# Kernel tuning notes

Hardware: AMD Instinct MI355X
Metric: run time of the kernel (lower is better)

## Reference

```python
import jax, jax.numpy as jnp
import numpy as np

ND, NT, B = 16384, 16384, 4096
FD, FT, C = 256, 256, 768


def _gat(x_src, x_dst, ei, Ws, Wd, a_s, a_d, b, num_dst, self_loops):
    """PyG GATConv, heads=1: per-edge attention softmax over incoming edges."""
    if self_loops:
        loops = jnp.arange(num_dst, dtype=ei.dtype)
        ei = jnp.concatenate([ei, jnp.stack([loops, loops])], axis=1)
    src, dst = ei[0], ei[1]
    hs = x_src @ Ws                                   # [Ns, C]
    hd = x_dst @ Wd                                   # [Ndst, C]
    e = jax.nn.leaky_relu((hs @ a_s)[src] + (hd @ a_d)[dst], 0.2)   # [E]
    m = jax.ops.segment_max(e, dst, num_segments=num_dst)
    p = jnp.exp(e - m[dst])
    s = jax.ops.segment_sum(p, dst, num_segments=num_dst)
    alpha = p / (s[dst] + 1e-16)
    out = jax.ops.segment_sum(hs[src] * alpha[:, None], dst, num_segments=num_dst)
    return out + b


def _l2norm(x):
    n = jnp.linalg.norm(x, axis=1, keepdims=True)
    return x / jnp.maximum(n, 1e-12)


def setup_inputs() -> dict:
    ks = iter(jax.random.split(jax.random.key(0), 64))
    def nrm(shape, fan_in=None):
        s = 1.0 if fan_in is None else (1.0 / fan_in) ** 0.5
        return jax.random.normal(next(ks), shape, jnp.float32) * s
    inp = {}
    inp["x_drug"] = nrm((ND, FD))
    inp["x_target"] = nrm((NT, FT))
    inp["cell_features"] = nrm((B, 890))
    for et, fs, fd in (("dd", FD, FD), ("dt", FD, FT), ("tt", FT, FT)):
        inp[f"W_src_{et}"] = nrm((fs, C), fs)
        inp[f"W_dst_{et}"] = nrm((fd, C), fd)
        inp[f"a_src_{et}"] = nrm((C,), C)
        inp[f"a_dst_{et}"] = nrm((C,), C)
        inp[f"b_{et}"] = jnp.zeros((C,), jnp.float32)
    for name, fi, fo in (("red1", 890, 2048), ("red2", 2048, 512), ("red3", 512, 2 * C),
                         ("r2a", 4 * C, 2048), ("r2b", 2048, 512), ("r2c", 512, C), ("cls", C, 2)):
        inp[f"{name}_w"] = nrm((fi, fo), fi)
        inp[f"{name}_b"] = jnp.zeros((fo,), jnp.float32)
    inp["drug1_id"] = jax.random.randint(next(ks), (B,), 0, ND)
    inp["drug2_id"] = jax.random.randint(next(ks), (B,), 0, ND)
    inp["ei_dd"] = jax.random.randint(next(ks), (2, 131072), 0, ND)
    inp["ei_dt"] = jnp.stack([jax.random.randint(next(ks), (262144,), 0, ND),
                              jax.random.randint(next(ks), (262144,), 0, NT)])
    inp["ei_tt"] = jax.random.randint(next(ks), (2, 262144), 0, NT)
    return inp


def reference(x_drug, x_target, cell_features,
              W_src_dd, W_dst_dd, a_src_dd, a_dst_dd, b_dd,
              W_src_dt, W_dst_dt, a_src_dt, a_dst_dt, b_dt,
              W_src_tt, W_dst_tt, a_src_tt, a_dst_tt, b_tt,
              red1_w, red1_b, red2_w, red2_b, red3_w, red3_b,
              r2a_w, r2a_b, r2b_w, r2b_b, r2c_w, r2c_b,
              cls_w, cls_b,
              drug1_id, drug2_id, ei_dd, ei_dt, ei_tt):
    # HeteroConv (aggr='sum') followed by per-type ReLU, num_layers=1
    drug = jax.nn.relu(_gat(x_drug, x_drug, ei_dd,
                            W_src_dd, W_dst_dd, a_src_dd, a_dst_dd, b_dd, ND, True))
    target = jax.nn.relu(
        _gat(x_drug, x_target, ei_dt, W_src_dt, W_dst_dt, a_src_dt, a_dst_dt, b_dt, NT, False)
        + _gat(x_target, x_target, ei_tt, W_src_tt, W_dst_tt, a_src_tt, a_dst_tt, b_tt, NT, True))
    del target  # with num_layers=1 the target embeddings never feed the output (faithful)
    d1 = drug[drug1_id]
    d2 = drug[drug2_id]
    cell = _l2norm(cell_features)
    cell = jax.nn.relu(cell @ red1_w + red1_b)
    cell = jax.nn.relu(cell @ red2_w + red2_b)
    cell = jax.nn.relu(cell @ red3_w + red3_b)          # [B, 2*C]
    hidden = _l2norm(jnp.concatenate([d1, d2, cell], axis=1))  # [B, 4*C]
    hidden = jax.nn.relu(hidden @ r2a_w + r2a_b)
    hidden = jax.nn.relu(hidden @ r2b_w + r2b_b)
    hidden = jax.nn.relu(hidden @ r2c_w + r2c_b)
    return hidden @ cls_w + cls_b                       # [B, 2]
```

## Files before the change

kernel.cpp:

```cpp
#include <hip/hip_runtime.h>
#include <cstdint>

#define ND 16384
#define BATCH 4096
#define CDIM 768
#define E_DD 131072
#define FD 256

typedef unsigned short u16;
typedef u16 u16x4 __attribute__((ext_vector_type(4)));
typedef u16 u16x8 __attribute__((ext_vector_type(8)));
typedef short s16x8 __attribute__((ext_vector_type(8)));
typedef float f32x4 __attribute__((ext_vector_type(4)));

__device__ __forceinline__ u16 f2bf(float x) {
  union { float f; uint32_t u; } v; v.f = x;
  uint32_t r = v.u + 0x7fffu + ((v.u >> 16) & 1u);
  return (u16)(r >> 16);
}
__device__ __forceinline__ float bf2f(u16 h) {
  union { float f; uint32_t u; } v; v.u = ((uint32_t)h) << 16;
  return v.f;
}
__device__ __forceinline__ uint32_t split2p(float x) {
  u16 h = f2bf(x);
  u16 l = f2bf(x - bf2f(h));
  return ((uint32_t)h << 16) | l;
}

#define KP 40

template <int KS, int OUT_BF16, int RELU, int BIAS, int ASPLIT, int ALO, int BLO>
__device__ __forceinline__ void gemm_core(
    int bx, int by, int bz,
    const float* __restrict__ Af,
    const u16* __restrict__ Ahi, const u16* __restrict__ Alo,
    const u16* __restrict__ Bhi, const u16* __restrict__ Blo,
    const float* __restrict__ bias,
    float* __restrict__ Cf, u16* __restrict__ Chi,
    int M, int N, int K, u16* AsB, u16* BsB) {
  constexpr int MT = 4, NT = 4;
  constexpr int BM = 128, BN = 128;
  constexpr int ASEG = BM / 64;
  constexpr int BSEG = BN / 64;

  const int t = threadIdx.x;
  const int bm0 = bx * BM, bn0 = by * BN;
  const int wid = t >> 6, lane = t & 63;
  const int quad = lane >> 4, l16 = lane & 15;
  const int wm0 = (wid >> 1) * (MT * 16);
  const int wn0 = (wid & 1) * (NT * 16);

  const int chunk = K / KS;
  const int kbeg = (KS > 1) ? bz * chunk : 0;
  const int kend = kbeg + chunk;

  auto As = [&](int a, int r, int k) -> u16& { return AsB[(a * BM + r) * KP + k]; };
  auto Bs = [&](int a, int r, int k) -> u16& { return BsB[(a * BN + r) * KP + k]; };

  f32x4 acc[MT][NT];
#pragma unroll
  for (int i = 0; i < MT; ++i)
#pragma unroll
    for (int j = 0; j < NT; ++j) acc[i][j] = (f32x4){0.f, 0.f, 0.f, 0.f};

  u16x8 pAh[ASEG], pAl[ASEG], pBh[BSEG], pBl[BSEG];

  auto loadA = [&](int c, int kk) {
    int s = t + 256 * c, row = s >> 2, kq = (s & 3) * 8;
    size_t off = (size_t)(bm0 + row) * K + kk + kq;
    if (ASPLIT) {
      f32x4 v0 = *(const f32x4*)(Af + off);
      f32x4 v1 = *(const f32x4*)(Af + off + 4);
      u16x8 h, l;
#pragma unroll
      for (int e = 0; e < 4; ++e) {
        uint32_t p = split2p(v0[e]);
        h[e] = (u16)(p >> 16); l[e] = (u16)(p & 0xffffu);
        uint32_t q = split2p(v1[e]);
        h[e + 4] = (u16)(q >> 16); l[e + 4] = (u16)(q & 0xffffu);
      }
      pAh[c] = h; pAl[c] = l;
    } else {
      pAh[c] = *(const u16x8*)(Ahi + off);
      if (ALO) pAl[c] = *(const u16x8*)(Alo + off);
    }
  };
  auto loadB = [&](int c, int kk) {
    int s = t + 256 * c, row = s >> 2, kq = (s & 3) * 8;
    size_t off = (size_t)(bn0 + row) * K + kk + kq;
    pBh[c] = *(const u16x8*)(Bhi + off);
    if (BLO) pBl[c] = *(const u16x8*)(Blo + off);
  };

#pragma unroll
  for (int c = 0; c < ASEG; ++c) loadA(c, kbeg);
#pragma unroll
  for (int c = 0; c < BSEG; ++c) loadB(c, kbeg);

  for (int k0 = kbeg;;) {
    __syncthreads();
#pragma unroll
    for (int c = 0; c < ASEG; ++c) {
      int s = t + 256 * c, row = s >> 2, kq = (s & 3) * 8;
      *(u16x8*)&As(0, row, kq) = pAh[c];
      if (ALO) *(u16x8*)&As(1, row, kq) = pAl[c];
    }
#pragma unroll
    for (int c = 0; c < BSEG; ++c) {
      int s = t + 256 * c, row = s >> 2, kq = (s & 3) * 8;
      *(u16x8*)&Bs(0, row, kq) = pBh[c];
      if (BLO) *(u16x8*)&Bs(1, row, kq) = pBl[c];
    }
    __syncthreads();

    int kn = k0 + 32;
    if (kn < kend) {
#pragma unroll
      for (int c = 0; c < ASEG; ++c) loadA(c, kn);
#pragma unroll
      for (int c = 0; c < BSEG; ++c) loadB(c, kn);
    }

    s16x8 ah[MT], al[MT], bh[NT], bl[NT];
#pragma unroll
    for (int mi = 0; mi < MT; ++mi) {
      ah[mi] = *(const s16x8*)&As(0, wm0 + mi * 16 + l16, quad * 8);
      if (ALO) al[mi] = *(const s16x8*)&As(1, wm0 + mi * 16 + l16, quad * 8);
    }
#pragma unroll
    for (int ni = 0; ni < NT; ++ni) {
      bh[ni] = *(const s16x8*)&Bs(0, wn0 + ni * 16 + l16, quad * 8);
      if (BLO) bl[ni] = *(const s16x8*)&Bs(1, wn0 + ni * 16 + l16, quad * 8);
    }
#pragma unroll
    for (int mi = 0; mi < MT; ++mi)
#pragma unroll
      for (int ni = 0; ni < NT; ++ni) {
        acc[mi][ni] = __builtin_amdgcn_mfma_f32_16x16x32_bf16(
            ah[mi], bh[ni], acc[mi][ni], 0, 0, 0);
        if (BLO)
          acc[mi][ni] = __builtin_amdgcn_mfma_f32_16x16x32_bf16(
              ah[mi], bl[ni], acc[mi][ni], 0, 0, 0);
        if (ALO)
          acc[mi][ni] = __builtin_amdgcn_mfma_f32_16x16x32_bf16(
              al[mi], bh[ni], acc[mi][ni], 0, 0, 0);
      }
    k0 = kn;
    if (k0 >= kend) break;
  }

  float* Cp = (KS > 1) ? Cf + (size_t)bz * M * N : Cf;
#pragma unroll
  for (int mi = 0; mi < MT; ++mi) {
#pragma unroll
    for (int ni = 0; ni < NT; ++ni) {
      int row = bm0 + wm0 + mi * 16 + quad * 4;
      int col = bn0 + wn0 + ni * 16 + l16;
      float bv = BIAS ? bias[col] : 0.f;
#pragma unroll
      for (int r = 0; r < 4; ++r) {
        float v = acc[mi][ni][r] + bv;
        if (RELU) v = fmaxf(v, 0.f);
        size_t o = (size_t)(row + r) * N + col;
        if (OUT_BF16) Chi[o] = f2bf(v);
        else Cp[o] = v;
      }
    }
  }
}

template <int KS, int OUT_BF16, int RELU, int BIAS, int ASPLIT, int ALO, int BLO>
__global__ __launch_bounds__(256) void mfma_gemm(
    const float* __restrict__ Af,
    const u16* __restrict__ Ahi, const u16* __restrict__ Alo,
    const u16* __restrict__ Bhi, const u16* __restrict__ Blo,
    const float* __restrict__ bias,
    float* __restrict__ Cf, u16* __restrict__ Chi,
    int M, int N, int K) {
  __shared__ __align__(16) u16 AsB[(ALO ? 2 : 1) * 128 * KP];
  __shared__ __align__(16) u16 BsB[(BLO ? 2 : 1) * 128 * KP];
  gemm_core<KS, OUT_BF16, RELU, BIAS, ASPLIT, ALO, BLO>(
      blockIdx.x, blockIdx.y, (KS > 1) ? (int)blockIdx.z : 0,
      Af, Ahi, Alo, Bhi, Blo, bias, Cf, Chi, M, N, K, AsB, BsB);
}

__device__ __forceinline__ void gat_body(
    int idx, const u16* __restrict__ hs, const float* __restrict__ es,
    const float* __restrict__ ed, const int* __restrict__ offsets,
    const int* __restrict__ slots, const float* __restrict__ bias,
    const int* __restrict__ d1, const int* __restrict__ d2,
    u16* __restrict__ out) {
  if (idx >= 2 * BATCH) return;
  int d = (idx < BATCH) ? d1[idx] : d2[idx - BATCH];
  int lane = threadIdx.x & 63;
  int beg = offsets[d], end = offsets[d + 1];
  float edv = ed[d];
  float mx = -1e30f;
  for (int j = beg + lane; j < end; j += 64) {
    float e = es[slots[j]] + edv;
    e = e >= 0.f ? e : 0.2f * e;
    mx = fmaxf(mx, e);
  }
#pragma unroll
  for (int m = 32; m; m >>= 1) mx = fmaxf(mx, __shfl_xor(mx, m));
  float sm = 0.f;
  for (int j = beg + lane; j < end; j += 64) {
    float e = es[slots[j]] + edv;
    e = e >= 0.f ? e : 0.2f * e;
    sm += expf(e - mx);
  }
#pragma unroll
  for (int m = 32; m; m >>= 1) sm += __shfl_xor(sm, m);
  float inv = 1.f / (sm + 1e-16f);
  int c8 = lane * 8;
  int c4 = 512 + lane * 4;
  float a8[8] = {};
  float a4[4] = {};
  for (int j = beg; j < end; ++j) {
    int srcn = slots[j];
    float e = es[srcn] + edv;
    e = e >= 0.f ? e : 0.2f * e;
    float alpha = expf(e - mx) * inv;
    const u16* hrow = hs + (size_t)srcn * CDIM;
    u16x8 r8 = *(const u16x8*)(hrow + c8);
    u16x4 r4 = *(const u16x4*)(hrow + c4);
#pragma unroll
    for (int e2 = 0; e2 < 8; ++e2) a8[e2] = fmaf(alpha, bf2f(r8[e2]), a8[e2]);
#pragma unroll
    for (int e2 = 0; e2 < 4; ++e2) a4[e2] = fmaf(alpha, bf2f(r4[e2]), a4[e2]);
  }
  u16* orow = out + (size_t)d * CDIM;
  u16x8 o8;
  u16x4 o4;
#pragma unroll
  for (int e2 = 0; e2 < 8; ++e2) o8[e2] = f2bf(fmaxf(a8[e2] + bias[c8 + e2], 0.f));
#pragma unroll
  for (int e2 = 0; e2 < 4; ++e2) o4[e2] = f2bf(fmaxf(a4[e2] + bias[c4 + e2], 0.f));
  *(u16x8*)(orow + c8) = o8;
  *(u16x4*)(orow + c4) = o4;
}

__global__ __launch_bounds__(256) void dual_gemm_red1_hs(
    const u16* __restrict__ cn, const u16* __restrict__ r1T,
    const float* __restrict__ red1_b, u16* __restrict__ c1,
    const float* __restrict__ xd, const u16* __restrict__ wsrcT,
    u16* __restrict__ hs) {
  __shared__ __align__(16) u16 AsB[2 * 128 * KP];
  __shared__ __align__(16) u16 BsB[128 * KP];
  int b = blockIdx.x;
  if (b < 512) {
    gemm_core<1, 1, 1, 1, 0, 0, 0>(b & 31, b >> 5, 0, nullptr, cn, nullptr,
                                   r1T, nullptr, red1_b, nullptr, c1,
                                   BATCH, 2048, 896, AsB, BsB);
  } else {
    int b2 = b - 512;
    gemm_core<1, 1, 0, 0, 1, 1, 0>(b2 & 127, b2 >> 7, 0, xd, nullptr, nullptr,
                                   wsrcT, nullptr, nullptr, nullptr, hs,
                                   ND, CDIM, FD, AsB, BsB);
  }
}

__global__ __launch_bounds__(256) void dual_red2_gat(
    const u16* __restrict__ c1, const u16* __restrict__ r2T,
    float* __restrict__ P,
    const u16* __restrict__ hs, const float* __restrict__ es,
    const float* __restrict__ ed, const int* __restrict__ offsets,
    const int* __restrict__ slots, const float* __restrict__ bias,
    const int* __restrict__ d1, const int* __restrict__ d2,
    u16* __restrict__ drug) {
  __shared__ __align__(16) u16 AsB[128 * KP];
  __shared__ __align__(16) u16 BsB[128 * KP];
  int b = blockIdx.x;
  if (b < 512) {
    gemm_core<4, 0, 0, 0, 0, 0, 0>(b & 31, (b >> 5) & 3, b >> 7, nullptr,
                                   c1, nullptr, r2T, nullptr, nullptr, P,
                                   nullptr, BATCH, 512, 2048, AsB, BsB);
  } else {
    int idx = (b - 512) * 4 + (threadIdx.x >> 6);
    gat_body(idx, hs, es, ed, offsets, slots, bias, d1, d2, drug);
  }
}

template <int KS>
__global__ void reduce_split_ks(const float* __restrict__ P,
                                const float* __restrict__ bias,
                                u16* __restrict__ Chi, int M, int N) {
  int i = blockIdx.x * 256 + threadIdx.x;
  int total = (M * N) >> 2;
  if (i >= total) return;
  f32x4 s = ((const f32x4*)P)[i];
#pragma unroll
  for (int z = 1; z < KS; ++z) s += ((const f32x4*)P)[(size_t)z * total + i];
  int col = (i * 4) % N;
  f32x4 bv = *(const f32x4*)(bias + col);
  u16x4 h;
#pragma unroll
  for (int e = 0; e < 4; ++e) h[e] = f2bf(fmaxf(s[e] + bv[e], 0.f));
  *(u16x4*)&Chi[i * 4] = h;
}

__global__ void reduce_cls(const float* __restrict__ P,
                           const float* __restrict__ bias,
                           const float* __restrict__ clsw,
                           const float* __restrict__ clsb,
                           float* __restrict__ out) {
  int row = blockIdx.x * 4 + (threadIdx.x >> 6);
  int lane = threadIdx.x & 63;
  const f32x4* p0 = (const f32x4*)(P + (size_t)row * CDIM);
  const f32x4* p1 = (const f32x4*)(P + (size_t)BATCH * CDIM + (size_t)row * CDIM);
  float s0 = 0.f, s1 = 0.f;
#pragma unroll
  for (int i = 0; i < 3; ++i) {
    int c4 = lane + 64 * i;
    f32x4 a = p0[c4] + p1[c4];
    f32x4 bv = *(const f32x4*)(bias + c4 * 4);
#pragma unroll
    for (int e = 0; e < 4; ++e) {
      float h = fmaxf(a[e] + bv[e], 0.f);
      int c = c4 * 4 + e;
      s0 = fmaf(h, clsw[c * 2 + 0], s0);
      s1 = fmaf(h, clsw[c * 2 + 1], s1);
    }
  }
#pragma unroll
  for (int m = 32; m; m >>= 1) {
    s0 += __shfl_xor(s0, m);
    s1 += __shfl_xor(s1, m);
  }
  if (lane == 0) {
    out[row * 2 + 0] = s0 + clsb[0];
    out[row * 2 + 1] = s1 + clsb[1];
  }
}

struct TDesc {
  const float* W;
  u16* Th;
  int K, N, Kpad, start;
};
struct TPack { TDesc d[7]; };

__global__ void multi_transpose(TPack p) {
  __shared__ float tile[32][33];
  int b = blockIdx.x;
  int mi = 0;
#pragma unroll
  for (int i = 1; i < 7; ++i)
    if (b >= p.d[i].start) mi = i;
  TDesc dd = p.d[mi];
  int rel = b - dd.start;
  int tilesX = dd.Kpad / 32;
  int k0 = (rel % tilesX) * 32, n0 = (rel / tilesX) * 32;
  int tx = threadIdx.x, ty = threadIdx.y;
#pragma unroll
  for (int i = 0; i < 4; ++i) {
    int k = k0 + ty + 8 * i, n = n0 + tx;
    tile[ty + 8 * i][tx] = (k < dd.K && n < dd.N) ? dd.W[(size_t)k * dd.N + n] : 0.f;
  }
  __syncthreads();
#pragma unroll
  for (int i = 0; i < 4; ++i) {
    int n = n0 + ty + 8 * i, k = k0 + tx;
    if (n < dd.N) dd.Th[(size_t)n * dd.Kpad + k] = f2bf(tile[tx][ty + 8 * i]);
  }
}

__global__ void wvec_kernel(const float* __restrict__ Wsrc,
                            const float* __restrict__ Wdst,
                            const float* __restrict__ a_s,
                            const float* __restrict__ a_d,
                            float* __restrict__ wsv, float* __restrict__ wdv) {
  int k = blockIdx.x;
  int t = threadIdx.x;
  __shared__ float rs[256], rd[256];
  float s = 0.f, d = 0.f;
  for (int c = t; c < CDIM; c += 256) {
    s += Wsrc[(size_t)k * CDIM + c] * a_s[c];
    d += Wdst[(size_t)k * CDIM + c] * a_d[c];
  }
  rs[t] = s; rd[t] = d;
  __syncthreads();
  for (int st = 128; st; st >>= 1) {
    if (t < st) { rs[t] += rs[t + st]; rd[t] += rd[t + st]; }
    __syncthreads();
  }
  if (t == 0) { wsv[k] = rs[0]; wdv[k] = rd[0]; }
}

__global__ void esed_kernel(const float* __restrict__ x,
                            const float* __restrict__ wsv,
                            const float* __restrict__ wdv,
                            float* __restrict__ es, float* __restrict__ ed,
                            int* __restrict__ counts) {
  if (blockIdx.x < 64) counts[blockIdx.x * 256 + threadIdx.x] = 1;
  int i = blockIdx.x * 256 + threadIdx.x;
  int lane = threadIdx.x & 63;
  int row = i >> 6;
  int c4 = lane * 4;
  f32x4 v = ((const f32x4*)x)[i];
  f32x4 ws = *(const f32x4*)(wsv + c4);
  f32x4 wd = *(const f32x4*)(wdv + c4);
  float a = v[0] * ws[0] + v[1] * ws[1] + v[2] * ws[2] + v[3] * ws[3];
  float b = v[0] * wd[0] + v[1] * wd[1] + v[2] * wd[2] + v[3] * wd[3];
#pragma unroll
  for (int m = 32; m; m >>= 1) {
    a += __shfl_xor(a, m);
    b += __shfl_xor(b, m);
  }
  if (lane == 0) { es[row] = a; ed[row] = b; }
}

__global__ void count_edges(const int* __restrict__ dst, int* counts) {
  int e = blockIdx.x * 256 + threadIdx.x;
  if (e < E_DD) atomicAdd(&counts[dst[e]], 1);
}
__global__ void scan_kernel(const int* __restrict__ counts, int* __restrict__ offsets,
                            int* __restrict__ cursor, int* __restrict__ slots) {
  __shared__ int part[512];
  int t = threadIdx.x;
  int base = t * 32;
  int s = 0;
  for (int i = 0; i < 32; ++i) s += counts[base + i];
  part[t] = s;
  __syncthreads();
  if (t == 0) {
    int run = 0;
    for (int i = 0; i < 512; ++i) { int tmp = part[i]; part[i] = run; run += tmp; }
    offsets[ND] = run;
  }
  __syncthreads();
  int run = part[t];
  for (int i = 0; i < 32; ++i) {
    int d = base + i;
    offsets[d] = run;
    slots[run] = d;
    cursor[d] = run + 1;
    run += counts[d];
  }
}
__global__ void scatter_edges(const int* __restrict__ src, const int* __restrict__ dst,
                              int* cursor, int* slots) {
  int e = blockIdx.x * 256 + threadIdx.x;
  if (e < E_DD) {
    int pos = atomicAdd(&cursor[dst[e]], 1);
    slots[pos] = src[e];
  }
}

__global__ void l2norm_bf16(const float* __restrict__ in, u16* __restrict__ hi,
                            int L, int Lp) {
  int row = blockIdx.x;
  int t = threadIdx.x;
  __shared__ float red[256];
  const float* irow = in + (size_t)row * L;
  float s = 0.f;
  for (int c = t; c < L; c += 256) { float v = irow[c]; s += v * v; }
  red[t] = s;
  __syncthreads();
  for (int st = 128; st; st >>= 1) {
    if (t < st) red[t] += red[t + st];
    __syncthreads();
  }
  float inv = 1.f / fmaxf(sqrtf(red[0]), 1e-12f);
  for (int c = t; c < Lp; c += 256) {
    float v = (c < L) ? irow[c] * inv : 0.f;
    hi[(size_t)row * Lp + c] = f2bf(v);
  }
}

__global__ __launch_bounds__(256) void hidden_build_bf16(
    const u16* __restrict__ drug, const u16* __restrict__ c3,
    const int* __restrict__ d1, const int* __restrict__ d2,
    u16* __restrict__ hhi) {
  int row = blockIdx.x;
  int t = threadIdx.x;
  const u16* s1 = drug + (size_t)d1[row] * CDIM;
  const u16* s2 = drug + (size_t)d2[row] * CDIM;
  const u16* s3 = c3 + (size_t)row * (2 * CDIM);
  float vals[12];
  float ss = 0.f;
#pragma unroll
  for (int i = 0; i < 12; ++i) {
    int c = t + 256 * i;
    float v;
    if (i < 3)      v = bf2f(s1[c]);
    else if (i < 6) v = bf2f(s2[c - CDIM]);
    else            v = bf2f(s3[c - 2 * CDIM]);
    vals[i] = v;
    ss += v * v;
  }
  __shared__ float red[256];
  red[t] = ss;
  __syncthreads();
  for (int st = 128; st; st >>= 1) {
    if (t < st) red[t] += red[t + st];
    __syncthreads();
  }
  float inv = 1.f / fmaxf(sqrtf(red[0]), 1e-12f);
  u16* hrow_h = hhi + (size_t)row * (4 * CDIM);
#pragma unroll
  for (int i = 0; i < 12; ++i) hrow_h[t + 256 * i] = f2bf(vals[i] * inv);
}

extern "C" void kernel_launch(void* const* d_in, const int* in_sizes, int n_in,
                              void* d_out, int out_size, void* d_ws, size_t ws_size,
                              hipStream_t stream) {
  const float* x_drug   = (const float*)d_in[0];
  const float* cellf    = (const float*)d_in[2];
  const float* W_src_dd = (const float*)d_in[3];
  const float* W_dst_dd = (const float*)d_in[4];
  const float* a_src_dd = (const float*)d_in[5];
  const float* a_dst_dd = (const float*)d_in[6];
  const float* b_dd     = (const float*)d_in[7];
  const float* red1_w = (const float*)d_in[18];
  const float* red1_b = (const float*)d_in[19];
  const float* red2_w = (const float*)d_in[20];
  const float* red2_b = (const float*)d_in[21];
  const float* red3_w = (const float*)d_in[22];
  const float* red3_b = (const float*)d_in[23];
  const float* r2a_w  = (const float*)d_in[24];
  const float* r2a_b  = (const float*)d_in[25];
  const float* r2b_w  = (const float*)d_in[26];
  const float* r2b_b  = (const float*)d_in[27];
  const float* r2c_w  = (const float*)d_in[28];
  const float* r2c_b  = (const float*)d_in[29];
  const float* cls_w  = (const float*)d_in[30];
  const float* cls_b  = (const float*)d_in[31];
  const int* drug1_id = (const int*)d_in[32];
  const int* drug2_id = (const int*)d_in[33];
  const int* ei_dd    = (const int*)d_in[34];
  float* out = (float*)d_out;

  const int* dd_src = ei_dd;
  const int* dd_dst = ei_dd + E_DD;

  char* w = (char*)d_ws;
  size_t off = 0;
  auto alloc = [&](size_t bytes) -> char* {
    char* p = w + off;
    off = (off + bytes + 255) & ~(size_t)255;
    return p;
  };
  u16* hs   = (u16*)alloc((size_t)ND * CDIM * 2);
  u16* drug = (u16*)alloc((size_t)ND * CDIM * 2);
  u16* c3   = (u16*)alloc((size_t)BATCH * 2 * CDIM * 2);
  float* P  = (float*)alloc((size_t)4 * BATCH * 512 * 4);
  u16* hid_hi = hs;
  u16* cn_hi = (u16*)alloc((size_t)BATCH * 896 * 2);
  u16* c1_hi = (u16*)alloc((size_t)BATCH * 2048 * 2);
  u16* c2_hi = (u16*)alloc((size_t)BATCH * 512 * 2);
  u16* wsrcT_hi = (u16*)alloc((size_t)CDIM * FD * 2);
  u16* r1T_hi = (u16*)alloc((size_t)2048 * 896 * 2);
  u16* r2T_hi = (u16*)alloc((size_t)512 * 2048 * 2);
  u16* r3T_hi = (u16*)alloc((size_t)1536 * 512 * 2);
  u16* raT_hi = (u16*)alloc((size_t)2048 * 3072 * 2);
  u16* rbT_hi = (u16*)alloc((size_t)512 * 2048 * 2);
  u16* rcT_hi = (u16*)alloc((size_t)768 * 512 * 2);
  float* es  = (float*)alloc((size_t)ND * 4);
  float* ed  = (float*)alloc((size_t)ND * 4);
  float* wsv = (float*)alloc(FD * 4);
  float* wdv = (float*)alloc(FD * 4);
  int* counts  = (int*)alloc((size_t)ND * 4);
  int* offsets = (int*)alloc((size_t)(ND + 1) * 4);
  int* cursor  = (int*)alloc((size_t)ND * 4);
  int* slots   = (int*)alloc((size_t)(E_DD + ND) * 4);
  (void)ws_size; (void)n_in; (void)in_sizes; (void)out_size;

  TPack tp;
  tp.d[0] = {W_src_dd, wsrcT_hi, 256, 768, 256, 0};
  tp.d[1] = {red1_w, r1T_hi, 890, 2048, 896, 192};
  tp.d[2] = {red2_w, r2T_hi, 2048, 512, 2048, 1984};
  tp.d[3] = {red3_w, r3T_hi, 512, 1536, 512, 3008};
  tp.d[4] = {r2a_w, raT_hi, 3072, 2048, 3072, 3776};
  tp.d[5] = {r2b_w, rbT_hi, 2048, 512, 2048, 9920};
  tp.d[6] = {r2c_w, rcT_hi, 512, 768, 512, 10944};
  multi_transpose<<<11328, dim3(32, 8), 0, stream>>>(tp);

  wvec_kernel<<<FD, 256, 0, stream>>>(W_src_dd, W_dst_dd, a_src_dd, a_dst_dd, wsv, wdv);
  esed_kernel<<<ND * FD / 1024, 256, 0, stream>>>(x_drug, wsv, wdv, es, ed, counts);
  count_edges<<<E_DD / 256, 256, 0, stream>>>(dd_dst, counts);
  scan_kernel<<<1, 512, 0, stream>>>(counts, offsets, cursor, slots);
  scatter_edges<<<E_DD / 256, 256, 0, stream>>>(dd_src, dd_dst, cursor, slots);
  l2norm_bf16<<<BATCH, 256, 0, stream>>>(cellf, cn_hi, 890, 896);

  dual_gemm_red1_hs<<<1280, 256, 0, stream>>>(cn_hi, r1T_hi, red1_b, c1_hi,
                                              x_drug, wsrcT_hi, hs);

  dual_red2_gat<<<512 + 2 * BATCH / 4, 256, 0, stream>>>(
      c1_hi, r2T_hi, P, hs, es, ed, offsets, slots, b_dd, drug1_id, drug2_id, drug);
  reduce_split_ks<4><<<BATCH * 512 / 1024, 256, 0, stream>>>(P, red2_b, c2_hi, BATCH, 512);
  mfma_gemm<1, 1, 1, 1, 0, 0, 0><<<dim3(BATCH / 128, 1536 / 128), 256, 0, stream>>>(
      nullptr, c2_hi, nullptr, r3T_hi, nullptr, red3_b, nullptr, c3, BATCH, 1536, 512);

  hidden_build_bf16<<<BATCH, 256, 0, stream>>>(drug, c3, drug1_id, drug2_id, hid_hi);

  mfma_gemm<1, 1, 1, 1, 0, 0, 0><<<dim3(BATCH / 128, 2048 / 128), 256, 0, stream>>>(
      nullptr, hid_hi, nullptr, raT_hi, nullptr, r2a_b, nullptr, c1_hi, BATCH, 2048, 3072);
  mfma_gemm<4, 0, 0, 0, 0, 0, 0><<<dim3(BATCH / 128, 512 / 128, 4), 256, 0, stream>>>(
      nullptr, c1_hi, nullptr, rbT_hi, nullptr, nullptr, P, nullptr, BATCH, 512, 2048);
  reduce_split_ks<4><<<BATCH * 512 / 1024, 256, 0, stream>>>(P, r2b_b, c2_hi, BATCH, 512);
  mfma_gemm<2, 0, 0, 0, 0, 0, 0><<<dim3(BATCH / 128, CDIM / 128, 2), 256, 0, stream>>>(
      nullptr, c2_hi, nullptr, rcT_hi, nullptr, nullptr, P, nullptr, BATCH, CDIM, 512);
  reduce_cls<<<BATCH / 4, 256, 0, stream>>>(P, r2c_b, cls_w, cls_b, out);
}
```

Measured before the change: 493.9 us.

## Deduplicate gathered drug ids for GAT and fuse small prep kernels

Marks which drug nodes are referenced by drug1_id/drug2_id, compacts them into a unique list with an atomic counter, and runs the GAT aggregation only once per unique node instead of once per batch slot. This removes duplicated edge softmax and aggregation work. It also merges several small launches: the wvec reduction into the transpose kernel, the esed and l2norm work into one kernel, and the edge count and scatter steps with the mask and compaction passes. The cost is extra mask/list buffers and atomics, and the GAT grid is still sized for the worst case, so idle waves exit early.

```diff
diff --git a/kernel.cpp b/kernel.cpp
--- a/kernel.cpp
+++ b/kernel.cpp
@@ -189,10 +189,10 @@
     int idx, const u16* __restrict__ hs, const float* __restrict__ es,
     const float* __restrict__ ed, const int* __restrict__ offsets,
     const int* __restrict__ slots, const float* __restrict__ bias,
-    const int* __restrict__ d1, const int* __restrict__ d2,
+    const int* __restrict__ list, const int* __restrict__ cnt,
     u16* __restrict__ out) {
-  if (idx >= 2 * BATCH) return;
-  int d = (idx < BATCH) ? d1[idx] : d2[idx - BATCH];
+  if (idx >= *cnt) return;
+  int d = list[idx];
   int lane = threadIdx.x & 63;
   int beg = offsets[d], end = offsets[d + 1];
   float edv = ed[d];
@@ -267,7 +267,7 @@
     const u16* __restrict__ hs, const float* __restrict__ es,
     const float* __restrict__ ed, const int* __restrict__ offsets,
     const int* __restrict__ slots, const float* __restrict__ bias,
-    const int* __restrict__ d1, const int* __restrict__ d2,
+    const int* __restrict__ list, const int* __restrict__ cnt,
     u16* __restrict__ drug) {
   __shared__ __align__(16) u16 AsB[128 * KP];
   __shared__ __align__(16) u16 BsB[128 * KP];
@@ -278,7 +278,7 @@
                                    nullptr, BATCH, 512, 2048, AsB, BsB);
   } else {
     int idx = (b - 512) * 4 + (threadIdx.x >> 6);
-    gat_body(idx, hs, es, ed, offsets, slots, bias, d1, d2, drug);
+    gat_body(idx, hs, es, ed, offsets, slots, bias, list, cnt, drug);
   }
 }
 
@@ -341,9 +341,30 @@
 };
 struct TPack { TDesc d[7]; };
 
-__global__ void multi_transpose(TPack p) {
+__global__ __launch_bounds__(256) void transpose_wvec(
+    TPack p, const float* __restrict__ Wsrc, const float* __restrict__ Wdst,
+    const float* __restrict__ a_s, const float* __restrict__ a_d,
+    float* __restrict__ wsv, float* __restrict__ wdv) {
   __shared__ float tile[32][33];
+  __shared__ float rs[256], rd[256];
   int b = blockIdx.x;
+  int t = threadIdx.x;
+  if (b >= 11328) {
+    int k = b - 11328;
+    float s = 0.f, d = 0.f;
+    for (int c = t; c < CDIM; c += 256) {
+      s += Wsrc[(size_t)k * CDIM + c] * a_s[c];
+      d += Wdst[(size_t)k * CDIM + c] * a_d[c];
+    }
+    rs[t] = s; rd[t] = d;
+    __syncthreads();
+    for (int st = 128; st; st >>= 1) {
+      if (t < st) { rs[t] += rs[t + st]; rd[t] += rd[t + st]; }
+      __syncthreads();
+    }
+    if (t == 0) { wsv[k] = rs[0]; wdv[k] = rd[0]; }
+    return;
+  }
   int mi = 0;
 #pragma unroll
   for (int i = 1; i < 7; ++i)
@@ -352,7 +373,7 @@
   int rel = b - dd.start;
   int tilesX = dd.Kpad / 32;
   int k0 = (rel % tilesX) * 32, n0 = (rel / tilesX) * 32;
-  int tx = threadIdx.x, ty = threadIdx.y;
+  int tx = t & 31, ty = t >> 5;
 #pragma unroll
   for (int i = 0; i < 4; ++i) {
     int k = k0 + ty + 8 * i, n = n0 + tx;
@@ -366,55 +387,70 @@
   }
 }
 
-__global__ void wvec_kernel(const float* __restrict__ Wsrc,
-                            const float* __restrict__ Wdst,
-                            const float* __restrict__ a_s,
-                            const float* __restrict__ a_d,
-                            float* __restrict__ wsv, float* __restrict__ wdv) {
-  int k = blockIdx.x;
+__global__ __launch_bounds__(256) void prep_act(
+    const float* __restrict__ x, const float* __restrict__ wsv,
+    const float* __restrict__ wdv, float* __restrict__ es,
+    float* __restrict__ ed, int* __restrict__ counts, int* __restrict__ mask,
+    int* __restrict__ cnt,
+    const float* __restrict__ cellf, u16* __restrict__ cn) {
+  __shared__ float red[256];
+  int b = blockIdx.x;
   int t = threadIdx.x;
-  __shared__ float rs[256], rd[256];
-  float s = 0.f, d = 0.f;
-  for (int c = t; c < CDIM; c += 256) {
-    s += Wsrc[(size_t)k * CDIM + c] * a_s[c];
-    d += Wdst[(size_t)k * CDIM + c] * a_d[c];
-  }
-  rs[t] = s; rd[t] = d;
-  __syncthreads();
-  for (int st = 128; st; st >>= 1) {
-    if (t < st) { rs[t] += rs[t + st]; rd[t] += rd[t + st]; }
+  if (b < 4096) {
+    if (b < 64) {
+      int i = b * 256 + t;
+      counts[i] = 1;
+      mask[i] = 0;
+      if (i == 0) *cnt = 0;
+    }
+    int i = b * 256 + t;
+    int lane = t & 63;
+    int row = i >> 6;
+    int c4 = lane * 4;
+    f32x4 v = ((const f32x4*)x)[i];
+    f32x4 ws = *(const f32x4*)(wsv + c4);
+    f32x4 wd = *(const f32x4*)(wdv + c4);
+    float a = v[0] * ws[0] + v[1] * ws[1] + v[2] * ws[2] + v[3] * ws[3];
+    float bb = v[0] * wd[0] + v[1] * wd[1] + v[2] * wd[2] + v[3] * wd[3];
+#pragma unroll
+    for (int m = 32; m; m >>= 1) {
+      a += __shfl_xor(a, m);
+      bb += __shfl_xor(bb, m);
+    }
+    if (lane == 0) { es[row] = a; ed[row] = bb; }
+  } else {
+    int row = b - 4096;
+    const float* irow = cellf + (size_t)row * 890;
+    float s = 0.f;
+    for (int c = t; c < 890; c += 256) { float v = irow[c]; s += v * v; }
+    red[t] = s;
     __syncthreads();
-  }
-  if (t == 0) { wsv[k] = rs[0]; wdv[k] = rd[0]; }
-}
-
-__global__ void esed_kernel(const float* __restrict__ x,
-                            const float* __restrict__ wsv,
-                            const float* __restrict__ wdv,
-                            float* __restrict__ es, float* __restrict__ ed,
-                            int* __restrict__ counts) {
-  if (blockIdx.x < 64) counts[blockIdx.x * 256 + threadIdx.x] = 1;
-  int i = blockIdx.x * 256 + threadIdx.x;
-  int lane = threadIdx.x & 63;
-  int row = i >> 6;
-  int c4 = lane * 4;
-  f32x4 v = ((const f32x4*)x)[i];
-  f32x4 ws = *(const f32x4*)(wsv + c4);
-  f32x4 wd = *(const f32x4*)(wdv + c4);
-  float a = v[0] * ws[0] + v[1] * ws[1] + v[2] * ws[2] + v[3] * ws[3];
-  float b = v[0] * wd[0] + v[1] * wd[1] + v[2] * wd[2] + v[3] * wd[3];
-#pragma unroll
-  for (int m = 32; m; m >>= 1) {
-    a += __shfl_xor(a, m);
-    b += __shfl_xor(b, m);
-  }
-  if (lane == 0) { es[row] = a; ed[row] = b; }
-}
-
-__global__ void count_edges(const int* __restrict__ dst, int* counts) {
-  int e = blockIdx.x * 256 + threadIdx.x;
-  if (e < E_DD) atomicAdd(&counts[dst[e]], 1);
-}
+    for (int st = 128; st; st >>= 1) {
+      if (t < st) red[t] += red[t + st];
+      __syncthreads();
+    }
+    float inv = 1.f / fmaxf(sqrtf(red[0]), 1e-12f);
+    for (int c = t; c < 896; c += 256) {
+      float v = (c < 890) ? irow[c] * inv : 0.f;
+      cn[(size_t)row * 896 + c] = f2bf(v);
+    }
+  }
+}
+
+__global__ void count_mark(const int* __restrict__ dst, int* counts,
+                           const int* __restrict__ d1, const int* __restrict__ d2,
+                           int* mask) {
+  int b = blockIdx.x;
+  if (b < 512) {
+    int e = b * 256 + threadIdx.x;
+    atomicAdd(&counts[dst[e]], 1);
+  } else {
+    int i = (b - 512) * 256 + threadIdx.x;
+    mask[d1[i]] = 1;
+    mask[d2[i]] = 1;
+  }
+}
+
 __global__ void scan_kernel(const int* __restrict__ counts, int* __restrict__ offsets,
                             int* __restrict__ cursor, int* __restrict__ slots) {
   __shared__ int part[512];
@@ -439,33 +475,23 @@
     run += counts[d];
   }
 }
-__global__ void scatter_edges(const int* __restrict__ src, const int* __restrict__ dst,
-                              int* cursor, int* slots) {
-  int e = blockIdx.x * 256 + threadIdx.x;
-  if (e < E_DD) {
+
+__global__ void scatter_compact(const int* __restrict__ src,
+                                const int* __restrict__ dst,
+                                int* cursor, int* slots,
+                                const int* __restrict__ mask, int* cnt,
+                                int* list) {
+  int b = blockIdx.x;
+  if (b < 512) {
+    int e = b * 256 + threadIdx.x;
     int pos = atomicAdd(&cursor[dst[e]], 1);
     slots[pos] = src[e];
-  }
-}
-
-__global__ void l2norm_bf16(const float* __restrict__ in, u16* __restrict__ hi,
-                            int L, int Lp) {
-  int row = blockIdx.x;
-  int t = threadIdx.x;
-  __shared__ float red[256];
-  const float* irow = in + (size_t)row * L;
-  float s = 0.f;
-  for (int c = t; c < L; c += 256) { float v = irow[c]; s += v * v; }
-  red[t] = s;
-  __syncthreads();
-  for (int st = 128; st; st >>= 1) {
-    if (t < st) red[t] += red[t + st];
-    __syncthreads();
-  }
-  float inv = 1.f / fmaxf(sqrtf(red[0]), 1e-12f);
-  for (int c = t; c < Lp; c += 256) {
-    float v = (c < L) ? irow[c] * inv : 0.f;
-    hi[(size_t)row * Lp + c] = f2bf(v);
+  } else {
+    int i = (b - 512) * 256 + threadIdx.x;
+    if (i < ND && mask[i]) {
+      int pos = atomicAdd(cnt, 1);
+      list[pos] = i;
+    }
   }
 }
 
@@ -565,6 +591,9 @@
   int* offsets = (int*)alloc((size_t)(ND + 1) * 4);
   int* cursor  = (int*)alloc((size_t)ND * 4);
   int* slots   = (int*)alloc((size_t)(E_DD + ND) * 4);
+  int* mask    = (int*)alloc((size_t)ND * 4);
+  int* list    = (int*)alloc((size_t)ND * 4);
+  int* cnt     = (int*)alloc(256);
   (void)ws_size; (void)n_in; (void)in_sizes; (void)out_size;
 
   TPack tp;
@@ -575,20 +604,21 @@
   tp.d[4] = {r2a_w, raT_hi, 3072, 2048, 3072, 3776};
   tp.d[5] = {r2b_w, rbT_hi, 2048, 512, 2048, 9920};
   tp.d[6] = {r2c_w, rcT_hi, 512, 768, 512, 10944};
-  multi_transpose<<<11328, dim3(32, 8), 0, stream>>>(tp);
-
-  wvec_kernel<<<FD, 256, 0, stream>>>(W_src_dd, W_dst_dd, a_src_dd, a_dst_dd, wsv, wdv);
-  esed_kernel<<<ND * FD / 1024, 256, 0, stream>>>(x_drug, wsv, wdv, es, ed, counts);
-  count_edges<<<E_DD / 256, 256, 0, stream>>>(dd_dst, counts);
+  transpose_wvec<<<11328 + FD, 256, 0, stream>>>(
+      tp, W_src_dd, W_dst_dd, a_src_dd, a_dst_dd, wsv, wdv);
+
+  prep_act<<<8192, 256, 0, stream>>>(x_drug, wsv, wdv, es, ed, counts, mask, cnt,
+                                     cellf, cn_hi);
+  count_mark<<<528, 256, 0, stream>>>(dd_dst, counts, drug1_id, drug2_id, mask);
   scan_kernel<<<1, 512, 0, stream>>>(counts, offsets, cursor, slots);
-  scatter_edges<<<E_DD / 256, 256, 0, stream>>>(dd_src, dd_dst, cursor, slots);
-  l2norm_bf16<<<BATCH, 256, 0, stream>>>(cellf, cn_hi, 890, 896);
+  scatter_compact<<<576, 256, 0, stream>>>(dd_src, dd_dst, cursor, slots,
+                                           mask, cnt, list);
 
   dual_gemm_red1_hs<<<1280, 256, 0, stream>>>(cn_hi, r1T_hi, red1_b, c1_hi,
                                               x_drug, wsrcT_hi, hs);
 
-  dual_red2_gat<<<512 + 2 * BATCH / 4, 256, 0, stream>>>(
-      c1_hi, r2T_hi, P, hs, es, ed, offsets, slots, b_dd, drug1_id, drug2_id, drug);
+  dual_red2_gat<<<512 + 2048, 256, 0, stream>>>(
+      c1_hi, r2T_hi, P, hs, es, ed, offsets, slots, b_dd, list, cnt, drug);
   reduce_split_ks<4><<<BATCH * 512 / 1024, 256, 0, stream>>>(P, red2_b, c2_hi, BATCH, 512);
   mfma_gemm<1, 1, 1, 1, 0, 0, 0><<<dim3(BATCH / 128, 1536 / 128), 256, 0, stream>>>(
       nullptr, c2_hi, nullptr, r3T_hi, nullptr, red3_b, nullptr, c3, BATCH, 1536, 512);
```

Measured after the change: 483.6 us. -2.1%, faster.
